# Optimization experiments

Measured on AMD Instinct MI355X. Metric: run time of the kernel, lower is better.

Reference implementation:

```python
import jax, jax.numpy as jnp
from jax import lax
import numpy as np

B, T, I, H, C = 2048, 512, 46, 64, 8

def setup_inputs() -> dict:
    key = jax.random.key(0)
    ks = jax.random.split(key, 7)
    s_ih = 1.0 / np.sqrt(H)  # PyTorch GRU init scale ~ U(-1/sqrt(H), 1/sqrt(H)); use scaled normal
    return {
        "x": jax.random.normal(ks[0], (B, T, I), jnp.float32),
        "w_ih": jax.random.normal(ks[1], (3 * H, I), jnp.float32) * s_ih,
        "w_hh": jax.random.normal(ks[2], (3 * H, H), jnp.float32) * s_ih,
        "b_ih": jax.random.normal(ks[3], (3 * H,), jnp.float32) * s_ih,
        "b_hh": jax.random.normal(ks[4], (3 * H,), jnp.float32) * s_ih,
        "fc_w": jax.random.normal(ks[5], (C, H), jnp.float32) * (1.0 / np.sqrt(H)),
        "fc_b": jax.random.normal(ks[6], (C,), jnp.float32) * (1.0 / np.sqrt(H)),
    }

def reference(x, w_ih, w_hh, b_ih, b_hh, fc_w, fc_b):
    # x: [B, T, I]. PyTorch GRU gate order: r, z, n.
    Bv, Tv, _ = x.shape
    Hv = w_hh.shape[1]
    # Precompute input contributions for all timesteps: [B, T, 3H]
    gx = jnp.einsum('bti,gi->btg', x, w_ih) + b_ih
    gx_t = jnp.swapaxes(gx, 0, 1)  # [T, B, 3H] for scan

    def step(h, gxt):
        gh = h @ w_hh.T + b_hh  # [B, 3H]
        xr, xz, xn = jnp.split(gxt, 3, axis=-1)
        hr, hz, hn = jnp.split(gh, 3, axis=-1)
        r = jax.nn.sigmoid(xr + hr)
        z = jax.nn.sigmoid(xz + hz)
        n = jnp.tanh(xn + r * hn)
        h_new = (1.0 - z) * n + z * h
        return h_new, None

    h0 = jnp.zeros((Bv, Hv), x.dtype)
    h_last, _ = lax.scan(step, h0, gx_t)  # last hidden == output[:, -1, :]
    logits = h_last @ fc_w.T + fc_b  # [B, C]
    return jax.nn.softmax(logits, axis=1)
```

## Files before the change

### kernel.cpp

```cpp
#include <hip/hip_runtime.h>
#include <hip/hip_bf16.h>

#define TT 512
#define II 46
#define HH 64
#define GG 192
#define CC 8
#define RR 8
#define KP 128

typedef __attribute__((ext_vector_type(8))) _Float16 half8;
typedef __attribute__((ext_vector_type(4))) float float4v;

__device__ inline float fsigm(float xv) {
  return __builtin_amdgcn_rcpf(1.f + __expf(-xv));
}
__device__ inline float ftanh2(float xv) {
  float e = __expf(2.f * xv);
  return __builtin_fmaf(-2.f, __builtin_amdgcn_rcpf(1.f + e), 1.f);
}

__device__ inline void barrier_lds_only() {
  asm volatile("s_waitcnt lgkmcnt(0)" ::: "memory");
  __builtin_amdgcn_s_barrier();
  asm volatile("" ::: "memory");
}

__global__ void pack_w(const float* __restrict__ w_ih, const float* __restrict__ w_hh,
                       _Float16* __restrict__ wp) {
  int idx = blockIdx.x * 256 + threadIdx.x;
  int u = idx >> 7, k = idx & 127;
  float v = (k < HH) ? w_hh[u * HH + k]
                     : ((k < HH + II) ? w_ih[u * II + (k - HH)] : 0.f);
  wp[idx] = (_Float16)v;
}

__launch_bounds__(256, 1)
__global__ void gru_main(const float* __restrict__ x,
                         const float* __restrict__ b_ih, const float* __restrict__ b_hh,
                         const float* __restrict__ fc_w, const float* __restrict__ fc_b,
                         const _Float16* __restrict__ wp,
                         float* __restrict__ out) {
  __shared__ __align__(16) _Float16 hsf[2][2][64][8];
  __shared__ __align__(16) _Float16 xsf[3][2][64][8];
  __shared__ float hf[RR][HH + 1];
  __shared__ float fcw[CC * HH];
  __shared__ float fcbs[CC];
  __shared__ float lgts[RR][CC];

  const int tau = threadIdx.x;
  const int w4  = tau >> 6;
  const int l   = tau & 63;
  const int m16 = l & 15;
  const int kg  = l >> 4;
  const int row0 = blockIdx.x * RR;

  {
    _Float16* p = &hsf[0][0][0][0];
    for (int i = tau; i < 2 * 2 * 64 * 8; i += 256) p[i] = (_Float16)0.f;
    p = &xsf[0][0][0][0];
    for (int i = tau; i < 3 * 2 * 64 * 8; i += 256) p[i] = (_Float16)0.f;
  }

  const int u = 16 * w4 + m16;
  const float br  = b_ih[u] + b_hh[u];
  const float bz  = b_ih[64 + u] + b_hh[64 + u];
  const float bnx = b_ih[128 + u];
  const float bnh = b_hh[128 + u];

  half8 bf[3][4];
#pragma unroll
  for (int g = 0; g < 3; ++g) {
    const _Float16* bb = wp + (size_t)(64 * g + u) * KP + kg * 8;
#pragma unroll
    for (int s = 0; s < 4; ++s) bf[g][s] = *(const half8*)(bb + 32 * s);
  }

  const int sh  = w4 >> 1;
  const int kgp = (u >> 3) & 3;
  const int jp  = u & 7;

  const int r1 = tau / II, i1 = tau % II;
  const int m1 = (r1 >> 1) * 4 + (r1 & 1);
  const bool has2 = (tau + 256) < RR * II;
  const int e2 = tau + 256;
  const int r2 = has2 ? e2 / II : r1, i2 = has2 ? e2 % II : i1;
  const int m2 = (r2 >> 1) * 4 + (r2 & 1);
  const float* xp1 = x + (size_t)(row0 + r1) * TT * II + i1;
  const float* xp2 = x + (size_t)(row0 + r2) * TT * II + i2;
  const int s1 = i1 >> 5, kg1 = (i1 >> 3) & 3, j1 = i1 & 7;
  const int s2 = i2 >> 5, kg2 = (i2 >> 3) & 3, j2 = i2 & 7;

  auto stageX = [&](int buf, float va, float vb) {
    xsf[buf][s1][kg1 * 16 + m1][j1] = (_Float16)va;
    if (has2) xsf[buf][s2][kg2 * 16 + m2][j2] = (_Float16)vb;
  };

  float hreg[2] = {0.f, 0.f};

  float v0a = xp1[0],            v0b = has2 ? xp2[0] : 0.f;
  float v1a = xp1[II],           v1b = has2 ? xp2[II] : 0.f;
  float xc1 = xp1[2 * II],       xc2 = has2 ? xp2[2 * II] : 0.f;
  float xn1 = xp1[3 * II],       xn2 = has2 ? xp2[3 * II] : 0.f;
  __syncthreads();
  stageX(0, v0a, v0b);
  stageX(1, v1a, v1b);
  __syncthreads();

  float4v xr, xz, xnx;
  {
    half8 c0 = *(const half8*)&xsf[0][0][l][0];
    half8 c1 = *(const half8*)&xsf[0][1][l][0];
    float4v z4 = {0.f, 0.f, 0.f, 0.f};
    float4v bn4 = {bnx, bnx, bnx, bnx};
    xr  = __builtin_amdgcn_mfma_f32_16x16x32_f16(c0, bf[0][2], z4, 0, 0, 0);
    xr  = __builtin_amdgcn_mfma_f32_16x16x32_f16(c1, bf[0][3], xr, 0, 0, 0);
    xz  = __builtin_amdgcn_mfma_f32_16x16x32_f16(c0, bf[1][2], z4, 0, 0, 0);
    xz  = __builtin_amdgcn_mfma_f32_16x16x32_f16(c1, bf[1][3], xz, 0, 0, 0);
    xnx = __builtin_amdgcn_mfma_f32_16x16x32_f16(c0, bf[2][2], bn4, 0, 0, 0);
    xnx = __builtin_amdgcn_mfma_f32_16x16x32_f16(c1, bf[2][3], xnx, 0, 0, 0);
  }

  for (int t = 0; t < TT; ++t) {
    if (t + 2 < TT) stageX((t + 2) % 3, xc1, xc2);
    xc1 = xn1; xc2 = xn2;
    if (t + 4 < TT) {
      xn1 = xp1[(size_t)(t + 4) * II];
      if (has2) xn2 = xp2[(size_t)(t + 4) * II];
    }

    barrier_lds_only();
    const int cur = t & 1, nxt = cur ^ 1;
    half8 a0 = *(const half8*)&hsf[cur][0][l][0];
    half8 a1 = *(const half8*)&hsf[cur][1][l][0];

    float4v r01 = {br, br, br, br};
    float4v z01 = {bz, bz, bz, bz};
    float4v nh  = {bnh, bnh, bnh, bnh};
    r01 = __builtin_amdgcn_mfma_f32_16x16x32_f16(a0, bf[0][0], r01, 0, 0, 0);
    nh  = __builtin_amdgcn_mfma_f32_16x16x32_f16(a0, bf[2][0], nh, 0, 0, 0);
    z01 = __builtin_amdgcn_mfma_f32_16x16x32_f16(a0, bf[1][0], z01, 0, 0, 0);
    r01 = __builtin_amdgcn_mfma_f32_16x16x32_f16(a1, bf[0][1], r01, 0, 0, 0);
    nh  = __builtin_amdgcn_mfma_f32_16x16x32_f16(a1, bf[2][1], nh, 0, 0, 0);
    z01 = __builtin_amdgcn_mfma_f32_16x16x32_f16(a1, bf[1][1], z01, 0, 0, 0);

    float aR[2]  = {r01[0] + xr[0], r01[1] + xr[1]};
    float aZ[2]  = {z01[0] + xz[0], z01[1] + xz[1]};
    float aNH[2] = {nh[0], nh[1]};
    float aNX[2] = {xnx[0], xnx[1]};

    if (t + 1 < TT) {
      const int nb = (t + 1) % 3;
      half8 c0 = *(const half8*)&xsf[nb][0][l][0];
      half8 c1 = *(const half8*)&xsf[nb][1][l][0];
      float4v z4 = {0.f, 0.f, 0.f, 0.f};
      float4v bn4 = {bnx, bnx, bnx, bnx};
      xr  = __builtin_amdgcn_mfma_f32_16x16x32_f16(c0, bf[0][2], z4, 0, 0, 0);
      xr  = __builtin_amdgcn_mfma_f32_16x16x32_f16(c1, bf[0][3], xr, 0, 0, 0);
      xz  = __builtin_amdgcn_mfma_f32_16x16x32_f16(c0, bf[1][2], z4, 0, 0, 0);
      xz  = __builtin_amdgcn_mfma_f32_16x16x32_f16(c1, bf[1][3], xz, 0, 0, 0);
      xnx = __builtin_amdgcn_mfma_f32_16x16x32_f16(c0, bf[2][2], bn4, 0, 0, 0);
      xnx = __builtin_amdgcn_mfma_f32_16x16x32_f16(c1, bf[2][3], xnx, 0, 0, 0);
    }

#pragma unroll
    for (int i = 0; i < 2; ++i) {
      float rg = fsigm(aR[i]);
      float zg = fsigm(aZ[i]);
      float pre = __builtin_fmaf(rg, aNH[i], aNX[i]);
      float ng = ftanh2(pre);
      hreg[i] = __builtin_fmaf(zg, hreg[i] - ng, ng);
      hsf[nxt][sh][kgp * 16 + kg * 4 + i][jp] = (_Float16)hreg[i];
    }
  }

  hf[2 * kg + 0][u] = hreg[0];
  hf[2 * kg + 1][u] = hreg[1];
  fcw[tau] = fc_w[tau];
  fcw[tau + 256] = fc_w[tau + 256];
  if (tau < CC) fcbs[tau] = fc_b[tau];
  __syncthreads();
  if (tau < RR * CC) {
    int rr = tau >> 3, c = tau & 7;
    float acc = fcbs[c];
#pragma unroll
    for (int j = 0; j < HH; ++j) acc += hf[rr][j] * fcw[c * HH + j];
    lgts[rr][c] = acc;
  }
  __syncthreads();
  if (tau < RR * CC) {
    int rr = tau >> 3, c = tau & 7;
    float mx = lgts[rr][0];
#pragma unroll
    for (int j = 1; j < CC; ++j) mx = fmaxf(mx, lgts[rr][j]);
    float ssum = 0.f;
#pragma unroll
    for (int j = 0; j < CC; ++j) ssum += __expf(lgts[rr][j] - mx);
    out[(size_t)(row0 + rr) * CC + c] = __expf(lgts[rr][c] - mx) / ssum;
  }
}

extern "C" void kernel_launch(void* const* d_in, const int* in_sizes, int n_in,
                              void* d_out, int out_size, void* d_ws, size_t ws_size,
                              hipStream_t stream) {
  const float* x    = (const float*)d_in[0];
  const float* w_ih = (const float*)d_in[1];
  const float* w_hh = (const float*)d_in[2];
  const float* b_ih = (const float*)d_in[3];
  const float* b_hh = (const float*)d_in[4];
  const float* fc_w = (const float*)d_in[5];
  const float* fc_b = (const float*)d_in[6];

  _Float16* wp = (_Float16*)d_ws;

  pack_w<<<96, 256, 0, stream>>>(w_ih, w_hh, wp);
  gru_main<<<256, 256, 0, stream>>>(x, b_ih, b_hh, fc_w, fc_b, wp, (float*)d_out);
}
```

Baseline: 211.4 us.

## Halve GRU block to two waves, each computing two hidden-unit tiles per step

Cuts the per-block thread count from 256 to 128, so each wave handles two 16-unit tiles and the per-step barrier synchronises fewer waves. The x-projection MFMAs now feed straight into the recurrent accumulators, with the r/z biases folded into the x-side init. The n-gate weights and biases are pre-scaled by 2 to drop a multiply in tanh. The x staging buffer gets four slots and the time loop is unrolled by four with static buffer indices. In exchange, each wave does twice the MFMA and transcendental work per step, which lengthens the serial critical path.

Measured after the change: 338.1 us. 1.6x slower.

```diff
diff --git a/kernel.cpp b/kernel.cpp
--- a/kernel.cpp
+++ b/kernel.cpp
@@ -15,8 +15,8 @@
 __device__ inline float fsigm(float xv) {
   return __builtin_amdgcn_rcpf(1.f + __expf(-xv));
 }
-__device__ inline float ftanh2(float xv) {
-  float e = __expf(2.f * xv);
+__device__ inline float ftanh_pre2(float pre2) {
+  float e = __expf(pre2);
   return __builtin_fmaf(-2.f, __builtin_amdgcn_rcpf(1.f + e), 1.f);
 }
 
@@ -32,24 +32,25 @@
   int u = idx >> 7, k = idx & 127;
   float v = (k < HH) ? w_hh[u * HH + k]
                      : ((k < HH + II) ? w_ih[u * II + (k - HH)] : 0.f);
+  if (u >= 128) v *= 2.f;
   wp[idx] = (_Float16)v;
 }
 
-__launch_bounds__(256, 1)
+__launch_bounds__(128, 1)
 __global__ void gru_main(const float* __restrict__ x,
                          const float* __restrict__ b_ih, const float* __restrict__ b_hh,
                          const float* __restrict__ fc_w, const float* __restrict__ fc_b,
                          const _Float16* __restrict__ wp,
                          float* __restrict__ out) {
   __shared__ __align__(16) _Float16 hsf[2][2][64][8];
-  __shared__ __align__(16) _Float16 xsf[3][2][64][8];
+  __shared__ __align__(16) _Float16 xsf[4][2][64][8];
   __shared__ float hf[RR][HH + 1];
   __shared__ float fcw[CC * HH];
   __shared__ float fcbs[CC];
   __shared__ float lgts[RR][CC];
 
   const int tau = threadIdx.x;
-  const int w4  = tau >> 6;
+  const int w   = tau >> 6;
   const int l   = tau & 63;
   const int m16 = l & 15;
   const int kg  = l >> 4;
@@ -57,127 +58,162 @@
 
   {
     _Float16* p = &hsf[0][0][0][0];
-    for (int i = tau; i < 2 * 2 * 64 * 8; i += 256) p[i] = (_Float16)0.f;
+    for (int i = tau; i < 2 * 2 * 64 * 8; i += 128) p[i] = (_Float16)0.f;
     p = &xsf[0][0][0][0];
-    for (int i = tau; i < 3 * 2 * 64 * 8; i += 256) p[i] = (_Float16)0.f;
-  }
-
-  const int u = 16 * w4 + m16;
-  const float br  = b_ih[u] + b_hh[u];
-  const float bz  = b_ih[64 + u] + b_hh[64 + u];
-  const float bnx = b_ih[128 + u];
-  const float bnh = b_hh[128 + u];
-
-  half8 bf[3][4];
-#pragma unroll
-  for (int g = 0; g < 3; ++g) {
-    const _Float16* bb = wp + (size_t)(64 * g + u) * KP + kg * 8;
-#pragma unroll
-    for (int s = 0; s < 4; ++s) bf[g][s] = *(const half8*)(bb + 32 * s);
-  }
-
-  const int sh  = w4 >> 1;
-  const int kgp = (u >> 3) & 3;
-  const int jp  = u & 7;
-
-  const int r1 = tau / II, i1 = tau % II;
-  const int m1 = (r1 >> 1) * 4 + (r1 & 1);
-  const bool has2 = (tau + 256) < RR * II;
-  const int e2 = tau + 256;
-  const int r2 = has2 ? e2 / II : r1, i2 = has2 ? e2 % II : i1;
-  const int m2 = (r2 >> 1) * 4 + (r2 & 1);
-  const float* xp1 = x + (size_t)(row0 + r1) * TT * II + i1;
-  const float* xp2 = x + (size_t)(row0 + r2) * TT * II + i2;
-  const int s1 = i1 >> 5, kg1 = (i1 >> 3) & 3, j1 = i1 & 7;
-  const int s2 = i2 >> 5, kg2 = (i2 >> 3) & 3, j2 = i2 & 7;
-
-  auto stageX = [&](int buf, float va, float vb) {
-    xsf[buf][s1][kg1 * 16 + m1][j1] = (_Float16)va;
-    if (has2) xsf[buf][s2][kg2 * 16 + m2][j2] = (_Float16)vb;
-  };
-
-  float hreg[2] = {0.f, 0.f};
-
-  float v0a = xp1[0],            v0b = has2 ? xp2[0] : 0.f;
-  float v1a = xp1[II],           v1b = has2 ? xp2[II] : 0.f;
-  float xc1 = xp1[2 * II],       xc2 = has2 ? xp2[2 * II] : 0.f;
-  float xn1 = xp1[3 * II],       xn2 = has2 ? xp2[3 * II] : 0.f;
-  __syncthreads();
-  stageX(0, v0a, v0b);
-  stageX(1, v1a, v1b);
-  __syncthreads();
-
-  float4v xr, xz, xnx;
+    for (int i = tau; i < 4 * 2 * 64 * 8; i += 128) p[i] = (_Float16)0.f;
+  }
+
+  const int u0 = 32 * w + m16;
+  const int u1 = u0 + 16;
+  const float br0 = b_ih[u0] + b_hh[u0],       br1 = b_ih[u1] + b_hh[u1];
+  const float bz0 = b_ih[64 + u0] + b_hh[64 + u0], bz1 = b_ih[64 + u1] + b_hh[64 + u1];
+  const float bnx0 = 2.f * b_ih[128 + u0],     bnx1 = 2.f * b_ih[128 + u1];
+  const float bnh0 = 2.f * b_hh[128 + u0],     bnh1 = 2.f * b_hh[128 + u1];
+
+  half8 Bh[2][3][2], Bx[2][3][2];
+#pragma unroll
+  for (int tl = 0; tl < 2; ++tl) {
+    const int uu = u0 + 16 * tl;
+#pragma unroll
+    for (int g = 0; g < 3; ++g) {
+      const _Float16* p = wp + (size_t)(64 * g + uu) * KP + 8 * kg;
+      Bh[tl][g][0] = *(const half8*)(p);
+      Bh[tl][g][1] = *(const half8*)(p + 32);
+      Bx[tl][g][0] = *(const half8*)(p + 64);
+      Bx[tl][g][1] = *(const half8*)(p + 96);
+    }
+  }
+
+  const int kgp0 = m16 >> 3;
+  const int jp   = m16 & 7;
+
+  bool ev_[3]; int es_[3], eln_[3], ej_[3];
+  const float* ep_[3];
+#pragma unroll
+  for (int q = 0; q < 3; ++q) {
+    int e = tau + 128 * q;
+    ev_[q] = e < RR * II;
+    int e2 = ev_[q] ? e : 0;
+    int b = e2 / II, i = e2 % II;
+    es_[q] = i >> 5;
+    eln_[q] = ((i >> 3) & 3) * 16 + (b >> 1) * 4 + (b & 1);
+    ej_[q] = i & 7;
+    ep_[q] = x + (size_t)(row0 + b) * TT * II + i;
+  }
+
+  float hreg[2][2] = {{0.f, 0.f}, {0.f, 0.f}};
+
+  float p0_[3], p1_[3], xc_[3], xn_[3];
+#pragma unroll
+  for (int q = 0; q < 3; ++q) {
+    p0_[q] = ev_[q] ? ep_[q][0] : 0.f;
+    p1_[q] = ev_[q] ? ep_[q][II] : 0.f;
+    xc_[q] = ev_[q] ? ep_[q][2 * II] : 0.f;
+    xn_[q] = ev_[q] ? ep_[q][3 * II] : 0.f;
+  }
+  __syncthreads();
+#pragma unroll
+  for (int q = 0; q < 3; ++q) if (ev_[q]) xsf[0][es_[q]][eln_[q]][ej_[q]] = (_Float16)p0_[q];
+#pragma unroll
+  for (int q = 0; q < 3; ++q) if (ev_[q]) xsf[1][es_[q]][eln_[q]][ej_[q]] = (_Float16)p1_[q];
+  __syncthreads();
+
+  float4v xaA[2][3], xaB[2][3];
   {
     half8 c0 = *(const half8*)&xsf[0][0][l][0];
     half8 c1 = *(const half8*)&xsf[0][1][l][0];
-    float4v z4 = {0.f, 0.f, 0.f, 0.f};
-    float4v bn4 = {bnx, bnx, bnx, bnx};
-    xr  = __builtin_amdgcn_mfma_f32_16x16x32_f16(c0, bf[0][2], z4, 0, 0, 0);
-    xr  = __builtin_amdgcn_mfma_f32_16x16x32_f16(c1, bf[0][3], xr, 0, 0, 0);
-    xz  = __builtin_amdgcn_mfma_f32_16x16x32_f16(c0, bf[1][2], z4, 0, 0, 0);
-    xz  = __builtin_amdgcn_mfma_f32_16x16x32_f16(c1, bf[1][3], xz, 0, 0, 0);
-    xnx = __builtin_amdgcn_mfma_f32_16x16x32_f16(c0, bf[2][2], bn4, 0, 0, 0);
-    xnx = __builtin_amdgcn_mfma_f32_16x16x32_f16(c1, bf[2][3], xnx, 0, 0, 0);
-  }
-
-  for (int t = 0; t < TT; ++t) {
-    if (t + 2 < TT) stageX((t + 2) % 3, xc1, xc2);
-    xc1 = xn1; xc2 = xn2;
-    if (t + 4 < TT) {
-      xn1 = xp1[(size_t)(t + 4) * II];
-      if (has2) xn2 = xp2[(size_t)(t + 4) * II];
-    }
-
+    const float brv[2] = {br0, br1}, bzv[2] = {bz0, bz1}, bxv[2] = {bnx0, bnx1};
+#pragma unroll
+    for (int tl = 0; tl < 2; ++tl) {
+      float4v r4 = {brv[tl], brv[tl], brv[tl], brv[tl]};
+      float4v z4 = {bzv[tl], bzv[tl], bzv[tl], bzv[tl]};
+      float4v n4 = {bxv[tl], bxv[tl], bxv[tl], bxv[tl]};
+      r4 = __builtin_amdgcn_mfma_f32_16x16x32_f16(c0, Bx[tl][0][0], r4, 0, 0, 0);
+      z4 = __builtin_amdgcn_mfma_f32_16x16x32_f16(c0, Bx[tl][1][0], z4, 0, 0, 0);
+      n4 = __builtin_amdgcn_mfma_f32_16x16x32_f16(c0, Bx[tl][2][0], n4, 0, 0, 0);
+      r4 = __builtin_amdgcn_mfma_f32_16x16x32_f16(c1, Bx[tl][0][1], r4, 0, 0, 0);
+      z4 = __builtin_amdgcn_mfma_f32_16x16x32_f16(c1, Bx[tl][1][1], z4, 0, 0, 0);
+      n4 = __builtin_amdgcn_mfma_f32_16x16x32_f16(c1, Bx[tl][2][1], n4, 0, 0, 0);
+      xaA[tl][0] = r4; xaA[tl][1] = z4; xaA[tl][2] = n4;
+    }
+  }
+
+  auto iter = [&](int t, int cur, int nb, int sb,
+                  float4v (&xaC)[2][3], float4v (&xaN)[2][3]) {
     barrier_lds_only();
-    const int cur = t & 1, nxt = cur ^ 1;
+    const int nxt = cur ^ 1;
     half8 a0 = *(const half8*)&hsf[cur][0][l][0];
     half8 a1 = *(const half8*)&hsf[cur][1][l][0];
-
-    float4v r01 = {br, br, br, br};
-    float4v z01 = {bz, bz, bz, bz};
-    float4v nh  = {bnh, bnh, bnh, bnh};
-    r01 = __builtin_amdgcn_mfma_f32_16x16x32_f16(a0, bf[0][0], r01, 0, 0, 0);
-    nh  = __builtin_amdgcn_mfma_f32_16x16x32_f16(a0, bf[2][0], nh, 0, 0, 0);
-    z01 = __builtin_amdgcn_mfma_f32_16x16x32_f16(a0, bf[1][0], z01, 0, 0, 0);
-    r01 = __builtin_amdgcn_mfma_f32_16x16x32_f16(a1, bf[0][1], r01, 0, 0, 0);
-    nh  = __builtin_amdgcn_mfma_f32_16x16x32_f16(a1, bf[2][1], nh, 0, 0, 0);
-    z01 = __builtin_amdgcn_mfma_f32_16x16x32_f16(a1, bf[1][1], z01, 0, 0, 0);
-
-    float aR[2]  = {r01[0] + xr[0], r01[1] + xr[1]};
-    float aZ[2]  = {z01[0] + xz[0], z01[1] + xz[1]};
-    float aNH[2] = {nh[0], nh[1]};
-    float aNX[2] = {xnx[0], xnx[1]};
-
-    if (t + 1 < TT) {
-      const int nb = (t + 1) % 3;
-      half8 c0 = *(const half8*)&xsf[nb][0][l][0];
-      half8 c1 = *(const half8*)&xsf[nb][1][l][0];
-      float4v z4 = {0.f, 0.f, 0.f, 0.f};
-      float4v bn4 = {bnx, bnx, bnx, bnx};
-      xr  = __builtin_amdgcn_mfma_f32_16x16x32_f16(c0, bf[0][2], z4, 0, 0, 0);
-      xr  = __builtin_amdgcn_mfma_f32_16x16x32_f16(c1, bf[0][3], xr, 0, 0, 0);
-      xz  = __builtin_amdgcn_mfma_f32_16x16x32_f16(c0, bf[1][2], z4, 0, 0, 0);
-      xz  = __builtin_amdgcn_mfma_f32_16x16x32_f16(c1, bf[1][3], xz, 0, 0, 0);
-      xnx = __builtin_amdgcn_mfma_f32_16x16x32_f16(c0, bf[2][2], bn4, 0, 0, 0);
-      xnx = __builtin_amdgcn_mfma_f32_16x16x32_f16(c1, bf[2][3], xnx, 0, 0, 0);
-    }
-
-#pragma unroll
-    for (int i = 0; i < 2; ++i) {
-      float rg = fsigm(aR[i]);
-      float zg = fsigm(aZ[i]);
-      float pre = __builtin_fmaf(rg, aNH[i], aNX[i]);
-      float ng = ftanh2(pre);
-      hreg[i] = __builtin_fmaf(zg, hreg[i] - ng, ng);
-      hsf[nxt][sh][kgp * 16 + kg * 4 + i][jp] = (_Float16)hreg[i];
-    }
-  }
-
-  hf[2 * kg + 0][u] = hreg[0];
-  hf[2 * kg + 1][u] = hreg[1];
+    half8 c0 = *(const half8*)&xsf[nb][0][l][0];
+    half8 c1 = *(const half8*)&xsf[nb][1][l][0];
+
+    float4v ar[2], az[2], an[2];
+    const float bnhv[2] = {bnh0, bnh1};
+#pragma unroll
+    for (int tl = 0; tl < 2; ++tl) {
+      float4v nh4 = {bnhv[tl], bnhv[tl], bnhv[tl], bnhv[tl]};
+      ar[tl] = __builtin_amdgcn_mfma_f32_16x16x32_f16(a0, Bh[tl][0][0], xaC[tl][0], 0, 0, 0);
+      az[tl] = __builtin_amdgcn_mfma_f32_16x16x32_f16(a0, Bh[tl][1][0], xaC[tl][1], 0, 0, 0);
+      an[tl] = __builtin_amdgcn_mfma_f32_16x16x32_f16(a0, Bh[tl][2][0], nh4, 0, 0, 0);
+      ar[tl] = __builtin_amdgcn_mfma_f32_16x16x32_f16(a1, Bh[tl][0][1], ar[tl], 0, 0, 0);
+      az[tl] = __builtin_amdgcn_mfma_f32_16x16x32_f16(a1, Bh[tl][1][1], az[tl], 0, 0, 0);
+      an[tl] = __builtin_amdgcn_mfma_f32_16x16x32_f16(a1, Bh[tl][2][1], an[tl], 0, 0, 0);
+    }
+
+    const float brv[2] = {br0, br1}, bzv[2] = {bz0, bz1}, bxv[2] = {bnx0, bnx1};
+#pragma unroll
+    for (int tl = 0; tl < 2; ++tl) {
+      float4v r4 = {brv[tl], brv[tl], brv[tl], brv[tl]};
+      float4v z4 = {bzv[tl], bzv[tl], bzv[tl], bzv[tl]};
+      float4v n4 = {bxv[tl], bxv[tl], bxv[tl], bxv[tl]};
+      r4 = __builtin_amdgcn_mfma_f32_16x16x32_f16(c0, Bx[tl][0][0], r4, 0, 0, 0);
+      z4 = __builtin_amdgcn_mfma_f32_16x16x32_f16(c0, Bx[tl][1][0], z4, 0, 0, 0);
+      n4 = __builtin_amdgcn_mfma_f32_16x16x32_f16(c0, Bx[tl][2][0], n4, 0, 0, 0);
+      r4 = __builtin_amdgcn_mfma_f32_16x16x32_f16(c1, Bx[tl][0][1], r4, 0, 0, 0);
+      z4 = __builtin_amdgcn_mfma_f32_16x16x32_f16(c1, Bx[tl][1][1], z4, 0, 0, 0);
+      n4 = __builtin_amdgcn_mfma_f32_16x16x32_f16(c1, Bx[tl][2][1], n4, 0, 0, 0);
+      xaN[tl][0] = r4; xaN[tl][1] = z4; xaN[tl][2] = n4;
+    }
+
+#pragma unroll
+    for (int q = 0; q < 3; ++q)
+      if (ev_[q]) xsf[sb][es_[q]][eln_[q]][ej_[q]] = (_Float16)xc_[q];
+#pragma unroll
+    for (int q = 0; q < 3; ++q) xc_[q] = xn_[q];
+    if (t + 4 < TT) {
+#pragma unroll
+      for (int q = 0; q < 3; ++q)
+        if (ev_[q]) xn_[q] = ep_[q][(size_t)(t + 4) * II];
+    }
+
+#pragma unroll
+    for (int tl = 0; tl < 2; ++tl) {
+#pragma unroll
+      for (int i = 0; i < 2; ++i) {
+        float rg = fsigm(ar[tl][i]);
+        float zg = fsigm(az[tl][i]);
+        float ng = ftanh_pre2(__builtin_fmaf(rg, an[tl][i], xaC[tl][2][i]));
+        hreg[tl][i] = __builtin_fmaf(zg, hreg[tl][i] - ng, ng);
+        hsf[nxt][w][(kgp0 + 2 * tl) * 16 + 4 * kg + i][jp] = (_Float16)hreg[tl][i];
+      }
+    }
+  };
+
+  for (int t = 0; t < TT; t += 4) {
+    iter(t,     0, 1, 2, xaA, xaB);
+    iter(t + 1, 1, 2, 3, xaB, xaA);
+    iter(t + 2, 0, 3, 0, xaA, xaB);
+    iter(t + 3, 1, 0, 1, xaB, xaA);
+  }
+
+  hf[2 * kg + 0][u0] = hreg[0][0];
+  hf[2 * kg + 1][u0] = hreg[0][1];
+  hf[2 * kg + 0][u1] = hreg[1][0];
+  hf[2 * kg + 1][u1] = hreg[1][1];
   fcw[tau] = fc_w[tau];
+  fcw[tau + 128] = fc_w[tau + 128];
   fcw[tau + 256] = fc_w[tau + 256];
+  fcw[tau + 384] = fc_w[tau + 384];
   if (tau < CC) fcbs[tau] = fc_b[tau];
   __syncthreads();
   if (tau < RR * CC) {
@@ -214,5 +250,5 @@
   _Float16* wp = (_Float16*)d_ws;
 
   pack_w<<<96, 256, 0, stream>>>(w_ih, w_hh, wp);
-  gru_main<<<256, 256, 0, stream>>>(x, b_ih, b_hh, fc_w, fc_b, wp, (float*)d_out);
-}
+  gru_main<<<256, 128, 0, stream>>>(x, b_ih, b_hh, fc_w, fc_b, wp, (float*)d_out);
+}
```
